# Optimization experiments

Hardware: AMD Instinct MI355X
Metric: run time of the kernel (lower is better)

Reference implementation:

```python
import jax, jax.numpy as jnp
import numpy as np

N_NODES = 50000
N_EDGES = 800000
IN_DIM = 128
HID = 128
BN_EPS = 1e-5


def _linear_init(key, fan_in, fan_out):
    kw, kb = jax.random.split(key)
    bound = 1.0 / np.sqrt(fan_in)
    w = jax.random.uniform(kw, (fan_in, fan_out), minval=-bound, maxval=bound, dtype=jnp.float32)
    b = jax.random.uniform(kb, (fan_out,), minval=-bound, maxval=bound, dtype=jnp.float32)
    return w, b


def setup_inputs() -> dict:
    key = jax.random.key(0)
    ks = jax.random.split(key, 8)
    x = jax.random.normal(ks[0], (N_NODES, IN_DIM), dtype=jnp.float32)
    edge_index = jax.random.randint(ks[1], (2, N_EDGES), 0, N_NODES, dtype=jnp.int32)
    # GIN layer 0 MLP: Linear(IN_DIM,HID) -> ReLU -> Linear(HID,HID)
    w0a, b0a = _linear_init(ks[2], IN_DIM, HID)
    w0b, b0b = _linear_init(ks[3], HID, HID)
    # GIN layer 1 MLP
    w1a, b1a = _linear_init(ks[4], HID, HID)
    w1b, b1b = _linear_init(ks[5], HID, HID)
    # encoder BatchNorm affine params (torch init: gamma=1, beta=0)
    bn_gamma = jnp.ones((HID,), jnp.float32)
    bn_beta = jnp.zeros((HID,), jnp.float32)
    # projection head: Linear(HID,HID) -> BatchNorm -> PReLU -> Dropout
    pw, pb = _linear_init(ks[6], HID, HID)
    pbn_gamma = jnp.ones((HID,), jnp.float32)
    pbn_beta = jnp.zeros((HID,), jnp.float32)
    prelu_a = jnp.asarray(0.25, jnp.float32)  # torch PReLU default init
    return {
        'x': x, 'edge_index': edge_index,
        'w0a': w0a, 'b0a': b0a, 'w0b': w0b, 'b0b': b0b,
        'w1a': w1a, 'b1a': b1a, 'w1b': w1b, 'b1b': b1b,
        'bn_gamma': bn_gamma, 'bn_beta': bn_beta,
        'pw': pw, 'pb': pb, 'pbn_gamma': pbn_gamma, 'pbn_beta': pbn_beta,
        'prelu_a': prelu_a,
    }


def _batch_norm(x, gamma, beta):
    # training-mode BatchNorm1d: biased variance over the node (batch) dim
    mu = jnp.mean(x, axis=0)
    var = jnp.var(x, axis=0)
    return gamma * (x - mu) * jax.lax.rsqrt(var + BN_EPS) + beta


def _gin_conv(z, src, dst, wa, ba, wb, bb):
    # sum-aggregate neighbor features: out[i] = (1+eps)*z[i] + sum_{j->i} z[j], eps=0
    agg = jax.ops.segment_sum(z[src], dst, num_segments=N_NODES)
    h = z + agg
    h = jax.nn.relu(h @ wa + ba)
    return h @ wb + bb


def reference(x, edge_index, w0a, b0a, w0b, b0b, w1a, b1a, w1b, b1b,
              bn_gamma, bn_beta, pw, pb, pbn_gamma, pbn_beta, prelu_a):
    src, dst = edge_index[0], edge_index[1]
    z = x
    z = jax.nn.relu(_gin_conv(z, src, dst, w0a, b0a, w0b, b0b))  # dropout: identity (deterministic)
    z = jax.nn.relu(_gin_conv(z, src, dst, w1a, b1a, w1b, b1b))
    z = _batch_norm(z, bn_gamma, bn_beta)
    p = z @ pw + pb
    p = _batch_norm(p, pbn_gamma, pbn_beta)
    p = jnp.where(p > 0, p, prelu_a * p)  # PReLU, single shared parameter
    return z, p
```

## Files before the change

kernel.cpp:

```cpp
#include <hip/hip_runtime.h>
#include <hip/hip_bf16.h>

#define NN 50000
#define NE 800000
#define HD 128
#define BN_EPS 1e-5f
#define MSTR 132
#define NBUK 782
#define PB 200
#define CHUNK 4000

typedef __attribute__((ext_vector_type(8))) __bf16 bf16x8;
typedef __attribute__((ext_vector_type(4))) __bf16 bf16x4;
typedef __attribute__((ext_vector_type(4))) float floatx4;

__global__ void k_zero_f(float* __restrict__ p, int n) {
    const int i = blockIdx.x * 256 + threadIdx.x;
    if (i < n) p[i] = 0.f;
}
__global__ void k_zero_i(int* __restrict__ p, int n) {
    const int i = blockIdx.x * 256 + threadIdx.x;
    if (i < n) p[i] = 0;
}

__global__ __launch_bounds__(256) void k_cast(const float* __restrict__ X,
                                              __bf16* __restrict__ Y) {
    const int i8 = (blockIdx.x * 256 + threadIdx.x) * 8;
    const float4 a = *(const float4*)&X[i8];
    const float4 b = *(const float4*)&X[i8 + 4];
    bf16x8 o;
    o[0] = (__bf16)a.x; o[1] = (__bf16)a.y; o[2] = (__bf16)a.z; o[3] = (__bf16)a.w;
    o[4] = (__bf16)b.x; o[5] = (__bf16)b.y; o[6] = (__bf16)b.z; o[7] = (__bf16)b.w;
    *(bf16x8*)&Y[i8] = o;
}

__global__ void k_wprep(const float* __restrict__ W0, const float* __restrict__ W1,
                        const float* __restrict__ W2, const float* __restrict__ W3,
                        const float* __restrict__ W4,
                        __bf16* __restrict__ Bh, __bf16* __restrict__ Bl) {
    const int n = blockIdx.x, m = blockIdx.y, k = threadIdx.x;
    const float* W = (m == 0) ? W0 : (m == 1) ? W1 : (m == 2) ? W2 : (m == 3) ? W3 : W4;
    const float w = W[k * HD + n];
    const __bf16 h = (__bf16)w;
    const int ct = n >> 4, lm = n & 15;
    const int ks = k >> 5, lq = (k & 31) >> 3, j = k & 7;
    const int lane = lq * 16 + lm;
    const size_t o = (size_t)m * HD * HD + (size_t)(((ct * 4 + ks) * 64) + lane) * 8 + j;
    Bh[o] = h;
    Bl[o] = (__bf16)(w - (float)h);
}


__global__ __launch_bounds__(256) void k_bcount(const int* __restrict__ dst,
                                                int* __restrict__ gbtot) {
    __shared__ int h[NBUK];
    for (int i = threadIdx.x; i < NBUK; i += 256) h[i] = 0;
    __syncthreads();
    const int e0 = blockIdx.x * CHUNK;
    for (int i = threadIdx.x; i < CHUNK; i += 256)
        atomicAdd(&h[dst[e0 + i] >> 6], 1);
    __syncthreads();
    for (int i = threadIdx.x; i < NBUK; i += 256) {
        const int v = h[i];
        if (v) atomicAdd(&gbtot[i], v);
    }
}

__global__ __launch_bounds__(256) void k_bscan(const int* __restrict__ gbtot,
                                               int* __restrict__ bbase,
                                               int* __restrict__ gcur,
                                               int* __restrict__ rowptr) {
    __shared__ int sh[256];
    const int t = threadIdx.x;
    int v[4];
    int s = 0;
#pragma unroll
    for (int j = 0; j < 4; ++j) {
        const int idx = t * 4 + j;
        v[j] = (idx < NBUK) ? gbtot[idx] : 0;
        s += v[j];
    }
    sh[t] = s;
    __syncthreads();
#pragma unroll
    for (int st = 1; st < 256; st <<= 1) {
        int add = (t >= st) ? sh[t - st] : 0;
        __syncthreads();
        sh[t] += add;
        __syncthreads();
    }
    int run = sh[t] - s;
#pragma unroll
    for (int j = 0; j < 4; ++j) {
        const int idx = t * 4 + j;
        if (idx < NBUK) { bbase[idx] = run; gcur[idx] = run; }
        run += v[j];
    }
    if (t == 255) bbase[NBUK] = run;
    if (t == 0) rowptr[NN] = NE;
}

__global__ __launch_bounds__(256) void k_bscatter(const int* __restrict__ src,
                                                  const int* __restrict__ dst,
                                                  int* __restrict__ gcur,
                                                  int2* __restrict__ pairs) {
    __shared__ int h[NBUK];
    __shared__ int cur[NBUK];
    for (int i = threadIdx.x; i < NBUK; i += 256) h[i] = 0;
    __syncthreads();
    const int e0 = blockIdx.x * CHUNK;
    for (int i = threadIdx.x; i < CHUNK; i += 256)
        atomicAdd(&h[dst[e0 + i] >> 6], 1);
    __syncthreads();
    for (int i = threadIdx.x; i < NBUK; i += 256) {
        const int v = h[i];
        if (v) cur[i] = atomicAdd(&gcur[i], v);
    }
    __syncthreads();
    for (int i = threadIdx.x; i < CHUNK; i += 256) {
        const int d = dst[e0 + i];
        const int pos = atomicAdd(&cur[d >> 6], 1);
        pairs[pos] = make_int2(src[e0 + i], d);
    }
}

__global__ __launch_bounds__(256) void k_csrfin(const int2* __restrict__ pairs,
                                                const int* __restrict__ bbase,
                                                int* __restrict__ rowptr,
                                                int* __restrict__ esrc) {
    __shared__ int cnt[64], lof[64], cur[64];
    const int b = blockIdx.x;
    const int s = bbase[b], e = bbase[b + 1];
    const int tid = threadIdx.x;
    if (tid < 64) cnt[tid] = 0;
    __syncthreads();
    for (int i = s + tid; i < e; i += 256)
        atomicAdd(&cnt[pairs[i].y & 63], 1);
    __syncthreads();
    if (tid == 0) {
        int r = 0;
#pragma unroll
        for (int j = 0; j < 64; ++j) { lof[j] = r; cur[j] = r; r += cnt[j]; }
    }
    __syncthreads();
    if (tid < 64) {
        const int node = b * 64 + tid;
        if (node < NN) rowptr[node] = s + lof[tid];
    }
    for (int i = s + tid; i < e; i += 256) {
        const int2 p = pairs[i];
        const int pos = atomicAdd(&cur[p.y & 63], 1);
        esrc[s + pos] = p.x;
    }
}

__device__ __forceinline__ void split8(const float4 a, const float4 b,
                                       bf16x8& hi, bf16x8& lo) {
    hi[0] = (__bf16)a.x; lo[0] = (__bf16)(a.x - (float)hi[0]);
    hi[1] = (__bf16)a.y; lo[1] = (__bf16)(a.y - (float)hi[1]);
    hi[2] = (__bf16)a.z; lo[2] = (__bf16)(a.z - (float)hi[2]);
    hi[3] = (__bf16)a.w; lo[3] = (__bf16)(a.w - (float)hi[3]);
    hi[4] = (__bf16)b.x; lo[4] = (__bf16)(b.x - (float)hi[4]);
    hi[5] = (__bf16)b.y; lo[5] = (__bf16)(b.y - (float)hi[5]);
    hi[6] = (__bf16)b.z; lo[6] = (__bf16)(b.z - (float)hi[6]);
    hi[7] = (__bf16)b.w; lo[7] = (__bf16)(b.w - (float)hi[7]);
}

__device__ __forceinline__ void addb8(float4& a, float4& b, const bf16x8 v) {
    a.x += (float)v[0]; a.y += (float)v[1]; a.z += (float)v[2]; a.w += (float)v[3];
    b.x += (float)v[4]; b.y += (float)v[5]; b.z += (float)v[6]; b.w += (float)v[7];
}

__global__ __launch_bounds__(256) void k_aggb(const __bf16* __restrict__ Z,
                                              const int* __restrict__ rowptr,
                                              const int* __restrict__ esrc,
                                              float* __restrict__ H) {
    const int g = threadIdx.x >> 4;
    const int lg = threadIdx.x & 15;
    const int node = blockIdx.x * 16 + g;
    const int cb = lg * 8;
    const int start = rowptr[node], end = rowptr[node + 1];
    float4 a = {0.f, 0.f, 0.f, 0.f}, b = {0.f, 0.f, 0.f, 0.f};
    addb8(a, b, *(const bf16x8*)&Z[(size_t)node * HD + cb]);
    int k = start;
    for (; k + 8 <= end; k += 8) {
        const int s0 = esrc[k + 0], s1 = esrc[k + 1];
        const int s2 = esrc[k + 2], s3 = esrc[k + 3];
        const int s4 = esrc[k + 4], s5 = esrc[k + 5];
        const int s6 = esrc[k + 6], s7 = esrc[k + 7];
        const bf16x8 v0 = *(const bf16x8*)&Z[(size_t)s0 * HD + cb];
        const bf16x8 v1 = *(const bf16x8*)&Z[(size_t)s1 * HD + cb];
        const bf16x8 v2 = *(const bf16x8*)&Z[(size_t)s2 * HD + cb];
        const bf16x8 v3 = *(const bf16x8*)&Z[(size_t)s3 * HD + cb];
        const bf16x8 v4 = *(const bf16x8*)&Z[(size_t)s4 * HD + cb];
        const bf16x8 v5 = *(const bf16x8*)&Z[(size_t)s5 * HD + cb];
        const bf16x8 v6 = *(const bf16x8*)&Z[(size_t)s6 * HD + cb];
        const bf16x8 v7 = *(const bf16x8*)&Z[(size_t)s7 * HD + cb];
        addb8(a, b, v0); addb8(a, b, v1); addb8(a, b, v2); addb8(a, b, v3);
        addb8(a, b, v4); addb8(a, b, v5); addb8(a, b, v6); addb8(a, b, v7);
    }
    for (; k + 4 <= end; k += 4) {
        const int s0 = esrc[k + 0], s1 = esrc[k + 1];
        const int s2 = esrc[k + 2], s3 = esrc[k + 3];
        const bf16x8 v0 = *(const bf16x8*)&Z[(size_t)s0 * HD + cb];
        const bf16x8 v1 = *(const bf16x8*)&Z[(size_t)s1 * HD + cb];
        const bf16x8 v2 = *(const bf16x8*)&Z[(size_t)s2 * HD + cb];
        const bf16x8 v3 = *(const bf16x8*)&Z[(size_t)s3 * HD + cb];
        addb8(a, b, v0); addb8(a, b, v1); addb8(a, b, v2); addb8(a, b, v3);
    }
    for (; k < end; ++k) {
        const int s = esrc[k];
        addb8(a, b, *(const bf16x8*)&Z[(size_t)s * HD + cb]);
    }
    *(float4*)&H[(size_t)node * HD + cb] = a;
    *(float4*)&H[(size_t)node * HD + cb + 4] = b;
}

__device__ __forceinline__ void mfma_pass(floatx4 (&acc)[8], const bf16x8 ah,
                                          const bf16x8 al, const __bf16* Bh,
                                          const __bf16* Bl, int ks, int lane) {
#pragma unroll
    for (int ct = 0; ct < 8; ++ct) {
        const size_t bo = (size_t)(((ct * 4 + ks) * 64) + lane) * 8;
        const bf16x8 bh = *(const bf16x8*)&Bh[bo];
        const bf16x8 bl = *(const bf16x8*)&Bl[bo];
        acc[ct] = __builtin_amdgcn_mfma_f32_16x16x32_bf16(al, bh, acc[ct], 0, 0, 0);
        acc[ct] = __builtin_amdgcn_mfma_f32_16x16x32_bf16(ah, bl, acc[ct], 0, 0, 0);
        acc[ct] = __builtin_amdgcn_mfma_f32_16x16x32_bf16(ah, bh, acc[ct], 0, 0, 0);
    }
}

template <int STATS, int OUT16>
__global__ __launch_bounds__(256) void k_mlp(const float* __restrict__ A,
                                             const __bf16* __restrict__ Bh1,
                                             const __bf16* __restrict__ Bl1,
                                             const float* __restrict__ b1,
                                             const __bf16* __restrict__ Bh2,
                                             const __bf16* __restrict__ Bl2,
                                             const float* __restrict__ b2,
                                             float* __restrict__ C,
                                             __bf16* __restrict__ C16,
                                             float* __restrict__ gsum,
                                             float* __restrict__ gsq) {
    __shared__ float mid[4][16 * MSTR];
    __shared__ float ssum[128], ssq[128];
    const int tid = threadIdx.x;
    const int wid = tid >> 6, lane = tid & 63;
    const int lq = lane >> 4, lm = lane & 15;
    if (STATS) {
        if (tid < 128) { ssum[tid] = 0.f; ssq[tid] = 0.f; }
        __syncthreads();
    }
    const int rowbase = blockIdx.x * 64 + wid * 16;
    const int r0 = min(rowbase + lm, NN - 1);
    float* m = &mid[wid][0];

    floatx4 acc[8];
#pragma unroll
    for (int j = 0; j < 8; ++j) acc[j] = (floatx4){0.f, 0.f, 0.f, 0.f};
#pragma unroll
    for (int ks = 0; ks < 4; ++ks) {
        const int kk = ks * 32 + lq * 8;
        const float4 aa = *(const float4*)&A[(size_t)r0 * HD + kk];
        const float4 ab = *(const float4*)&A[(size_t)r0 * HD + kk + 4];
        bf16x8 ah, al;
        split8(aa, ab, ah, al);
        mfma_pass(acc, ah, al, Bh1, Bl1, ks, lane);
    }
#pragma unroll
    for (int ct = 0; ct < 8; ++ct) {
        const int col = ct * 16 + lm;
        const float bcol = b1[col];
#pragma unroll
        for (int r = 0; r < 4; ++r)
            m[(lq * 4 + r) * MSTR + col] = fmaxf(acc[ct][r] + bcol, 0.f);
    }
#pragma unroll
    for (int j = 0; j < 8; ++j) acc[j] = (floatx4){0.f, 0.f, 0.f, 0.f};
#pragma unroll
    for (int ks = 0; ks < 4; ++ks) {
        const int kk = ks * 32 + lq * 8;
        const float4 aa = *(const float4*)&m[lm * MSTR + kk];
        const float4 ab = *(const float4*)&m[lm * MSTR + kk + 4];
        bf16x8 ah, al;
        split8(aa, ab, ah, al);
        mfma_pass(acc, ah, al, Bh2, Bl2, ks, lane);
    }
#pragma unroll
    for (int ct = 0; ct < 8; ++ct) {
        const int col = ct * 16 + lm;
        const float bcol = b2[col];
#pragma unroll
        for (int r = 0; r < 4; ++r)
            m[(lq * 4 + r) * MSTR + col] = fmaxf(acc[ct][r] + bcol, 0.f);
    }
    float s0 = 0.f, s1 = 0.f, s2 = 0.f, s3 = 0.f;
    float q0 = 0.f, q1 = 0.f, q2 = 0.f, q3 = 0.f;
    const int c0 = (lane * 4) & 127;
#pragma unroll
    for (int p = 0; p < 8; ++p) {
        const int idx = p * 256 + lane * 4;
        const int r = idx >> 7;
        const float4 v = *(const float4*)&m[r * MSTR + c0];
        const int row = rowbase + r;
        if (row < NN) {
            if (OUT16) {
                bf16x4 o;
                o[0] = (__bf16)v.x; o[1] = (__bf16)v.y;
                o[2] = (__bf16)v.z; o[3] = (__bf16)v.w;
                *(bf16x4*)&C16[(size_t)row * HD + c0] = o;
            } else {
                *(float4*)&C[(size_t)row * HD + c0] = v;
            }
            if (STATS) {
                s0 += v.x; q0 = fmaf(v.x, v.x, q0);
                s1 += v.y; q1 = fmaf(v.y, v.y, q1);
                s2 += v.z; q2 = fmaf(v.z, v.z, q2);
                s3 += v.w; q3 = fmaf(v.w, v.w, q3);
            }
        }
    }
    if (STATS) {
        s0 += __shfl_xor(s0, 32); q0 += __shfl_xor(q0, 32);
        s1 += __shfl_xor(s1, 32); q1 += __shfl_xor(q1, 32);
        s2 += __shfl_xor(s2, 32); q2 += __shfl_xor(q2, 32);
        s3 += __shfl_xor(s3, 32); q3 += __shfl_xor(q3, 32);
        if (lane < 32) {
            atomicAdd(&ssum[c0 + 0], s0); atomicAdd(&ssq[c0 + 0], q0);
            atomicAdd(&ssum[c0 + 1], s1); atomicAdd(&ssq[c0 + 1], q1);
            atomicAdd(&ssum[c0 + 2], s2); atomicAdd(&ssq[c0 + 2], q2);
            atomicAdd(&ssum[c0 + 3], s3); atomicAdd(&ssq[c0 + 3], q3);
        }
        __syncthreads();
        if (tid < 128) {
            atomicAdd(&gsum[tid], ssum[tid]);
            atomicAdd(&gsq[tid], ssq[tid]);
        }
    }
}

__global__ __launch_bounds__(256) void k_proj(const float* __restrict__ Z2,
                                              const float* __restrict__ bnsc,
                                              const float* __restrict__ bnsh,
                                              float* __restrict__ Zout,
                                              const __bf16* __restrict__ Bh,
                                              const __bf16* __restrict__ Bl,
                                              const float* __restrict__ bias,
                                              float* __restrict__ C,
                                              float* __restrict__ gsum,
                                              float* __restrict__ gsq) {
    __shared__ float tb[4][16 * MSTR];
    __shared__ float ssum[128], ssq[128];
    const int tid = threadIdx.x;
    const int wid = tid >> 6, lane = tid & 63;
    const int lq = lane >> 4, lm = lane & 15;
    if (tid < 128) { ssum[tid] = 0.f; ssq[tid] = 0.f; }
    __syncthreads();
    const int rowbase = blockIdx.x * 64 + wid * 16;
    const int r0 = min(rowbase + lm, NN - 1);
    const bool rowok = (rowbase + lm) < NN;
    float* m = &tb[wid][0];

    floatx4 acc[8];
#pragma unroll
    for (int j = 0; j < 8; ++j) acc[j] = (floatx4){0.f, 0.f, 0.f, 0.f};
#pragma unroll
    for (int ks = 0; ks < 4; ++ks) {
        const int kk = ks * 32 + lq * 8;
        const float4 za = *(const float4*)&Z2[(size_t)r0 * HD + kk];
        const float4 zb = *(const float4*)&Z2[(size_t)r0 * HD + kk + 4];
        const float4 sca = *(const float4*)&bnsc[kk];
        const float4 scb = *(const float4*)&bnsc[kk + 4];
        const float4 sha = *(const float4*)&bnsh[kk];
        const float4 shb = *(const float4*)&bnsh[kk + 4];
        float4 aa, ab;
        aa.x = fmaf(za.x, sca.x, sha.x); aa.y = fmaf(za.y, sca.y, sha.y);
        aa.z = fmaf(za.z, sca.z, sha.z); aa.w = fmaf(za.w, sca.w, sha.w);
        ab.x = fmaf(zb.x, scb.x, shb.x); ab.y = fmaf(zb.y, scb.y, shb.y);
        ab.z = fmaf(zb.z, scb.z, shb.z); ab.w = fmaf(zb.w, scb.w, shb.w);
        if (rowok) {
            *(float4*)&Zout[(size_t)r0 * HD + kk] = aa;
            *(float4*)&Zout[(size_t)r0 * HD + kk + 4] = ab;
        }
        bf16x8 ah, al;
        split8(aa, ab, ah, al);
        mfma_pass(acc, ah, al, Bh, Bl, ks, lane);
    }
#pragma unroll
    for (int ct = 0; ct < 8; ++ct) {
        const int col = ct * 16 + lm;
        const float bcol = bias[col];
#pragma unroll
        for (int r = 0; r < 4; ++r)
            m[(lq * 4 + r) * MSTR + col] = acc[ct][r] + bcol;
    }
    float s0 = 0.f, s1 = 0.f, s2 = 0.f, s3 = 0.f;
    float q0 = 0.f, q1 = 0.f, q2 = 0.f, q3 = 0.f;
    const int c0 = (lane * 4) & 127;
#pragma unroll
    for (int p = 0; p < 8; ++p) {
        const int idx = p * 256 + lane * 4;
        const int r = idx >> 7;
        const float4 v = *(const float4*)&m[r * MSTR + c0];
        const int row = rowbase + r;
        if (row < NN) {
            *(float4*)&C[(size_t)row * HD + c0] = v;
            s0 += v.x; q0 = fmaf(v.x, v.x, q0);
            s1 += v.y; q1 = fmaf(v.y, v.y, q1);
            s2 += v.z; q2 = fmaf(v.z, v.z, q2);
            s3 += v.w; q3 = fmaf(v.w, v.w, q3);
        }
    }
    s0 += __shfl_xor(s0, 32); q0 += __shfl_xor(q0, 32);
    s1 += __shfl_xor(s1, 32); q1 += __shfl_xor(q1, 32);
    s2 += __shfl_xor(s2, 32); q2 += __shfl_xor(q2, 32);
    s3 += __shfl_xor(s3, 32); q3 += __shfl_xor(q3, 32);
    if (lane < 32) {
        atomicAdd(&ssum[c0 + 0], s0); atomicAdd(&ssq[c0 + 0], q0);
        atomicAdd(&ssum[c0 + 1], s1); atomicAdd(&ssq[c0 + 1], q1);
        atomicAdd(&ssum[c0 + 2], s2); atomicAdd(&ssq[c0 + 2], q2);
        atomicAdd(&ssum[c0 + 3], s3); atomicAdd(&ssq[c0 + 3], q3);
    }
    __syncthreads();
    if (tid < 128) {
        atomicAdd(&gsum[tid], ssum[tid]);
        atomicAdd(&gsq[tid], ssq[tid]);
    }
}

__global__ void k_bnfin(const float* __restrict__ sum, const float* __restrict__ sumsq,
                        const float* __restrict__ gamma, const float* __restrict__ beta,
                        float* __restrict__ scale, float* __restrict__ shift) {
    const int c = threadIdx.x;
    const float mean = sum[c] * (1.f / NN);
    const float var = sumsq[c] * (1.f / NN) - mean * mean;
    const float sc = gamma[c] * rsqrtf(var + BN_EPS);
    scale[c] = sc;
    shift[c] = beta[c] - mean * sc;
}

__global__ void k_bnapply(const float* __restrict__ X, const float* __restrict__ scale,
                          const float* __restrict__ shift, float* __restrict__ Y,
                          const float* __restrict__ pa) {
    const int i4 = (blockIdx.x * 256 + threadIdx.x) * 4;
    const int c = i4 & 127;
    const float4 sc = *(const float4*)&scale[c];
    const float4 sh = *(const float4*)&shift[c];
    const float4 v = *(const float4*)&X[i4];
    float4 y;
    y.x = fmaf(v.x, sc.x, sh.x);
    y.y = fmaf(v.y, sc.y, sh.y);
    y.z = fmaf(v.z, sc.z, sh.z);
    y.w = fmaf(v.w, sc.w, sh.w);
    const float a = pa[0];
    if (y.x < 0.f) y.x *= a;
    if (y.y < 0.f) y.y *= a;
    if (y.z < 0.f) y.z *= a;
    if (y.w < 0.f) y.w *= a;
    *(float4*)&Y[i4] = y;
}

extern "C" void kernel_launch(void* const* d_in, const int* in_sizes, int n_in,
                              void* d_out, int out_size, void* d_ws, size_t ws_size,
                              hipStream_t stream) {
    const float* x = (const float*)d_in[0];
    const int* ei = (const int*)d_in[1];
    const float* w0a = (const float*)d_in[2];
    const float* b0a = (const float*)d_in[3];
    const float* w0b = (const float*)d_in[4];
    const float* b0b = (const float*)d_in[5];
    const float* w1a = (const float*)d_in[6];
    const float* b1a = (const float*)d_in[7];
    const float* w1b = (const float*)d_in[8];
    const float* b1b = (const float*)d_in[9];
    const float* bng = (const float*)d_in[10];
    const float* bnb = (const float*)d_in[11];
    const float* pw  = (const float*)d_in[12];
    const float* pb  = (const float*)d_in[13];
    const float* pbng = (const float*)d_in[14];
    const float* pbnb = (const float*)d_in[15];
    const float* pa = (const float*)d_in[16];

    float* outZ = (float*)d_out;
    float* outP = outZ + (size_t)NN * HD;

    float* ws = (float*)d_ws;
    float* bufH = ws;
    float* st = bufH + (size_t)NN * HD;
    int* rowptr = (int*)(st + 1024);
    int* esrc = rowptr + NN + 64;
    int* gbtot = esrc + NE;
    int* bbase = gbtot + 800;
    int* gcur = bbase + 800;
    __bf16* wth = (__bf16*)(gcur + 800);
    __bf16* wtl = wth + 5 * HD * HD;

    __bf16* xb  = (__bf16*)bufH;
    __bf16* z1b = xb + (size_t)NN * HD;
    int2* pairs = (int2*)z1b;
    float* Hbuf = outP;

    const int* srcv = ei;
    const int* dstv = ei + NE;

    const int ELV = (NN * HD) / (256 * 4);
    const int CVB = (NN * HD) / (256 * 8);
    const int GB = (NN + 63) / 64;
    const int AB = NN / 16;

    k_wprep<<<dim3(HD, 5), HD, 0, stream>>>(w0a, w0b, w1a, w1b, pw, wth, wtl);
    k_cast<<<CVB, 256, 0, stream>>>(x, xb);
    k_zero_f<<<4, 256, 0, stream>>>(st, 1024);
    k_zero_i<<<4, 256, 0, stream>>>(gbtot, 800);

    k_bcount<<<PB, 256, 0, stream>>>(dstv, gbtot);
    k_bscan<<<1, 256, 0, stream>>>(gbtot, bbase, gcur, rowptr);
    k_bscatter<<<PB, 256, 0, stream>>>(srcv, dstv, gcur, pairs);
    k_csrfin<<<NBUK, 256, 0, stream>>>(pairs, bbase, rowptr, esrc);

    k_aggb<<<AB, 256, 0, stream>>>(xb, rowptr, esrc, Hbuf);
    k_mlp<0, 1><<<GB, 256, 0, stream>>>(Hbuf,
                                        wth + 0 * HD * HD, wtl + 0 * HD * HD, b0a,
                                        wth + 1 * HD * HD, wtl + 1 * HD * HD, b0b,
                                        nullptr, z1b, nullptr, nullptr);

    k_aggb<<<AB, 256, 0, stream>>>(z1b, rowptr, esrc, Hbuf);
    k_mlp<1, 0><<<GB, 256, 0, stream>>>(Hbuf,
                                        wth + 2 * HD * HD, wtl + 2 * HD * HD, b1a,
                                        wth + 3 * HD * HD, wtl + 3 * HD * HD, b1b,
                                        outP, nullptr, st + 0, st + 128);

    k_bnfin<<<1, 128, 0, stream>>>(st + 0, st + 128, bng, bnb, st + 256, st + 384);
    k_proj<<<GB, 256, 0, stream>>>(outP, st + 256, st + 384, outZ,
                                   wth + 4 * HD * HD, wtl + 4 * HD * HD, pb,
                                   outP, st + 512, st + 640);

    k_bnfin<<<1, 128, 0, stream>>>(st + 512, st + 640, pbng, pbnb, st + 768, st + 896);
    k_bnapply<<<ELV, 256, 0, stream>>>(outP, st + 768, st + 896, outP, pa);
}
```

Before: 342.3 us.

## Split MLP GEMM columns across wave pairs, halving rows per block

The fused MLP and projection kernels now give each block 32 rows instead of 64. Two waves share each 16-row group, and each wave computes half of the 128 output columns with 4 accumulators instead of 8. The aim is to double the number of blocks and cut per-wave register and LDS use, which should improve occupancy and latency hiding. In exchange it adds block-wide barriers between the GEMM stages, and each wave re-reads the same A rows and re-does the bf16 split on them.

```diff
diff --git a/kernel.cpp b/kernel.cpp
--- a/kernel.cpp
+++ b/kernel.cpp
@@ -49,7 +49,6 @@
     Bh[o] = h;
     Bl[o] = (__bf16)(w - (float)h);
 }
-
 
 __global__ __launch_bounds__(256) void k_bcount(const int* __restrict__ dst,
                                                 int* __restrict__ gbtot) {
@@ -216,17 +215,18 @@
     *(float4*)&H[(size_t)node * HD + cb + 4] = b;
 }
 
-__device__ __forceinline__ void mfma_pass(floatx4 (&acc)[8], const bf16x8 ah,
-                                          const bf16x8 al, const __bf16* Bh,
-                                          const __bf16* Bl, int ks, int lane) {
-#pragma unroll
-    for (int ct = 0; ct < 8; ++ct) {
+__device__ __forceinline__ void mfma_pass4(floatx4 (&acc)[4], const bf16x8 ah,
+                                           const bf16x8 al, const __bf16* Bh,
+                                           const __bf16* Bl, int ks, int lane, int ch) {
+#pragma unroll
+    for (int c4 = 0; c4 < 4; ++c4) {
+        const int ct = ch * 4 + c4;
         const size_t bo = (size_t)(((ct * 4 + ks) * 64) + lane) * 8;
         const bf16x8 bh = *(const bf16x8*)&Bh[bo];
         const bf16x8 bl = *(const bf16x8*)&Bl[bo];
-        acc[ct] = __builtin_amdgcn_mfma_f32_16x16x32_bf16(al, bh, acc[ct], 0, 0, 0);
-        acc[ct] = __builtin_amdgcn_mfma_f32_16x16x32_bf16(ah, bl, acc[ct], 0, 0, 0);
-        acc[ct] = __builtin_amdgcn_mfma_f32_16x16x32_bf16(ah, bh, acc[ct], 0, 0, 0);
+        acc[c4] = __builtin_amdgcn_mfma_f32_16x16x32_bf16(al, bh, acc[c4], 0, 0, 0);
+        acc[c4] = __builtin_amdgcn_mfma_f32_16x16x32_bf16(ah, bl, acc[c4], 0, 0, 0);
+        acc[c4] = __builtin_amdgcn_mfma_f32_16x16x32_bf16(ah, bh, acc[c4], 0, 0, 0);
     }
 }
 
@@ -242,22 +242,22 @@
                                              __bf16* __restrict__ C16,
                                              float* __restrict__ gsum,
                                              float* __restrict__ gsq) {
-    __shared__ float mid[4][16 * MSTR];
+    __shared__ float mid[2][16 * MSTR];
     __shared__ float ssum[128], ssq[128];
     const int tid = threadIdx.x;
     const int wid = tid >> 6, lane = tid & 63;
     const int lq = lane >> 4, lm = lane & 15;
+    const int rg = wid >> 1, ch = wid & 1;
     if (STATS) {
         if (tid < 128) { ssum[tid] = 0.f; ssq[tid] = 0.f; }
-        __syncthreads();
-    }
-    const int rowbase = blockIdx.x * 64 + wid * 16;
+    }
+    const int rowbase = blockIdx.x * 32 + rg * 16;
     const int r0 = min(rowbase + lm, NN - 1);
-    float* m = &mid[wid][0];
-
-    floatx4 acc[8];
-#pragma unroll
-    for (int j = 0; j < 8; ++j) acc[j] = (floatx4){0.f, 0.f, 0.f, 0.f};
+    float* m = &mid[rg][0];
+
+    floatx4 acc[4];
+#pragma unroll
+    for (int j = 0; j < 4; ++j) acc[j] = (floatx4){0.f, 0.f, 0.f, 0.f};
 #pragma unroll
     for (int ks = 0; ks < 4; ++ks) {
         const int kk = ks * 32 + lq * 8;
@@ -265,18 +265,19 @@
         const float4 ab = *(const float4*)&A[(size_t)r0 * HD + kk + 4];
         bf16x8 ah, al;
         split8(aa, ab, ah, al);
-        mfma_pass(acc, ah, al, Bh1, Bl1, ks, lane);
-    }
-#pragma unroll
-    for (int ct = 0; ct < 8; ++ct) {
-        const int col = ct * 16 + lm;
+        mfma_pass4(acc, ah, al, Bh1, Bl1, ks, lane, ch);
+    }
+#pragma unroll
+    for (int c4 = 0; c4 < 4; ++c4) {
+        const int col = (ch * 4 + c4) * 16 + lm;
         const float bcol = b1[col];
 #pragma unroll
         for (int r = 0; r < 4; ++r)
-            m[(lq * 4 + r) * MSTR + col] = fmaxf(acc[ct][r] + bcol, 0.f);
-    }
-#pragma unroll
-    for (int j = 0; j < 8; ++j) acc[j] = (floatx4){0.f, 0.f, 0.f, 0.f};
+            m[(lq * 4 + r) * MSTR + col] = fmaxf(acc[c4][r] + bcol, 0.f);
+    }
+    __syncthreads();
+#pragma unroll
+    for (int j = 0; j < 4; ++j) acc[j] = (floatx4){0.f, 0.f, 0.f, 0.f};
 #pragma unroll
     for (int ks = 0; ks < 4; ++ks) {
         const int kk = ks * 32 + lq * 8;
@@ -284,22 +285,24 @@
         const float4 ab = *(const float4*)&m[lm * MSTR + kk + 4];
         bf16x8 ah, al;
         split8(aa, ab, ah, al);
-        mfma_pass(acc, ah, al, Bh2, Bl2, ks, lane);
-    }
-#pragma unroll
-    for (int ct = 0; ct < 8; ++ct) {
-        const int col = ct * 16 + lm;
+        mfma_pass4(acc, ah, al, Bh2, Bl2, ks, lane, ch);
+    }
+    __syncthreads();
+#pragma unroll
+    for (int c4 = 0; c4 < 4; ++c4) {
+        const int col = (ch * 4 + c4) * 16 + lm;
         const float bcol = b2[col];
 #pragma unroll
         for (int r = 0; r < 4; ++r)
-            m[(lq * 4 + r) * MSTR + col] = fmaxf(acc[ct][r] + bcol, 0.f);
-    }
+            m[(lq * 4 + r) * MSTR + col] = fmaxf(acc[c4][r] + bcol, 0.f);
+    }
+    __syncthreads();
     float s0 = 0.f, s1 = 0.f, s2 = 0.f, s3 = 0.f;
     float q0 = 0.f, q1 = 0.f, q2 = 0.f, q3 = 0.f;
     const int c0 = (lane * 4) & 127;
 #pragma unroll
-    for (int p = 0; p < 8; ++p) {
-        const int idx = p * 256 + lane * 4;
+    for (int p = 0; p < 4; ++p) {
+        const int idx = p * 512 + ch * 256 + lane * 4;
         const int r = idx >> 7;
         const float4 v = *(const float4*)&m[r * MSTR + c0];
         const int row = rowbase + r;
@@ -349,21 +352,21 @@
                                               float* __restrict__ C,
                                               float* __restrict__ gsum,
                                               float* __restrict__ gsq) {
-    __shared__ float tb[4][16 * MSTR];
+    __shared__ float tb[2][16 * MSTR];
     __shared__ float ssum[128], ssq[128];
     const int tid = threadIdx.x;
     const int wid = tid >> 6, lane = tid & 63;
     const int lq = lane >> 4, lm = lane & 15;
+    const int rg = wid >> 1, ch = wid & 1;
     if (tid < 128) { ssum[tid] = 0.f; ssq[tid] = 0.f; }
-    __syncthreads();
-    const int rowbase = blockIdx.x * 64 + wid * 16;
+    const int rowbase = blockIdx.x * 32 + rg * 16;
     const int r0 = min(rowbase + lm, NN - 1);
     const bool rowok = (rowbase + lm) < NN;
-    float* m = &tb[wid][0];
-
-    floatx4 acc[8];
-#pragma unroll
-    for (int j = 0; j < 8; ++j) acc[j] = (floatx4){0.f, 0.f, 0.f, 0.f};
+    float* m = &tb[rg][0];
+
+    floatx4 acc[4];
+#pragma unroll
+    for (int j = 0; j < 4; ++j) acc[j] = (floatx4){0.f, 0.f, 0.f, 0.f};
 #pragma unroll
     for (int ks = 0; ks < 4; ++ks) {
         const int kk = ks * 32 + lq * 8;
@@ -378,28 +381,29 @@
         aa.z = fmaf(za.z, sca.z, sha.z); aa.w = fmaf(za.w, sca.w, sha.w);
         ab.x = fmaf(zb.x, scb.x, shb.x); ab.y = fmaf(zb.y, scb.y, shb.y);
         ab.z = fmaf(zb.z, scb.z, shb.z); ab.w = fmaf(zb.w, scb.w, shb.w);
-        if (rowok) {
+        if (ch == 0 && rowok) {
             *(float4*)&Zout[(size_t)r0 * HD + kk] = aa;
             *(float4*)&Zout[(size_t)r0 * HD + kk + 4] = ab;
         }
         bf16x8 ah, al;
         split8(aa, ab, ah, al);
-        mfma_pass(acc, ah, al, Bh, Bl, ks, lane);
-    }
-#pragma unroll
-    for (int ct = 0; ct < 8; ++ct) {
-        const int col = ct * 16 + lm;
+        mfma_pass4(acc, ah, al, Bh, Bl, ks, lane, ch);
+    }
+#pragma unroll
+    for (int c4 = 0; c4 < 4; ++c4) {
+        const int col = (ch * 4 + c4) * 16 + lm;
         const float bcol = bias[col];
 #pragma unroll
         for (int r = 0; r < 4; ++r)
-            m[(lq * 4 + r) * MSTR + col] = acc[ct][r] + bcol;
-    }
+            m[(lq * 4 + r) * MSTR + col] = acc[c4][r] + bcol;
+    }
+    __syncthreads();
     float s0 = 0.f, s1 = 0.f, s2 = 0.f, s3 = 0.f;
     float q0 = 0.f, q1 = 0.f, q2 = 0.f, q3 = 0.f;
     const int c0 = (lane * 4) & 127;
 #pragma unroll
-    for (int p = 0; p < 8; ++p) {
-        const int idx = p * 256 + lane * 4;
+    for (int p = 0; p < 4; ++p) {
+        const int idx = p * 512 + ch * 256 + lane * 4;
         const int r = idx >> 7;
         const float4 v = *(const float4*)&m[r * MSTR + c0];
         const int row = rowbase + r;
@@ -505,7 +509,7 @@
 
     const int ELV = (NN * HD) / (256 * 4);
     const int CVB = (NN * HD) / (256 * 8);
-    const int GB = (NN + 63) / 64;
+    const int GB = (NN + 31) / 32;
     const int AB = NN / 16;
 
     k_wprep<<<dim3(HD, 5), HD, 0, stream>>>(w0a, w0b, w1a, w1b, pw, wth, wtl);
```

Measured after the change: 376.1 us. 1.1x slower.
